# Optimization experiments

Hardware: AMD Instinct MI355X
Metric: run time of the kernel (lower is better)

Reference implementation:

```python
import jax, jax.numpy as jnp
import numpy as np

MODEL_DIM = 2048
NUM_HEADS = 32
NUM_KV_HEADS = 8
HEAD_DIM = MODEL_DIM // NUM_HEADS  # 64
NUM_REP = NUM_HEADS // NUM_KV_HEADS  # 4


def setup_inputs() -> dict:
    key = jax.random.key(0)
    ks = jax.random.split(key, 6)
    B, S = 1, 2048
    s = 1.0 / np.sqrt(MODEL_DIM)
    x = jax.random.normal(ks[0], (B, S, MODEL_DIM), dtype=jnp.float32)
    # causal mask, 1 = keep, 0 = mask (scores.masked_fill(mask == 0, -1e9))
    mask = jnp.tril(jnp.ones((S, S), dtype=jnp.int32))[None, None, :, :]
    w_q = jax.random.normal(ks[1], (MODEL_DIM, MODEL_DIM), dtype=jnp.float32) * s
    w_k = jax.random.normal(ks[2], (NUM_KV_HEADS * HEAD_DIM, MODEL_DIM), dtype=jnp.float32) * s
    w_v = jax.random.normal(ks[3], (NUM_KV_HEADS * HEAD_DIM, MODEL_DIM), dtype=jnp.float32) * s
    w_o = jax.random.normal(ks[4], (MODEL_DIM, MODEL_DIM), dtype=jnp.float32) * s
    b_o = jax.random.normal(ks[5], (MODEL_DIM,), dtype=jnp.float32) * 0.01
    return {"x": x, "mask": mask, "w_q": w_q, "w_k": w_k, "w_v": w_v, "w_o": w_o, "b_o": b_o}


def reference(x, mask, w_q, w_k, w_v, w_o, b_o):
    B, S, _ = x.shape
    # projections (torch Linear: x @ W.T)
    q = (x @ w_q.T).reshape(B, S, NUM_HEADS, HEAD_DIM).transpose(0, 2, 1, 3)      # [B,H,S,D]
    k = (x @ w_k.T).reshape(B, S, NUM_KV_HEADS, HEAD_DIM).transpose(0, 2, 1, 3)   # [B,Hk,S,D]
    v = (x @ w_v.T).reshape(B, S, NUM_KV_HEADS, HEAD_DIM).transpose(0, 2, 1, 3)   # [B,Hk,S,D]
    # group Q heads by their shared KV head instead of materializing repeated KV
    qg = q.reshape(B, NUM_KV_HEADS, NUM_REP, S, HEAD_DIM)                         # [B,Hk,R,S,D]
    scale = 1.0 / np.sqrt(HEAD_DIM).astype(np.float32)
    scores = jnp.einsum('bgrsd,bgtd->bgrst', qg, k) * scale                       # [B,Hk,R,S,S]
    scores = jnp.where(mask[:, :, None, :, :] == 0, jnp.float32(-1e9), scores)
    attn = jax.nn.softmax(scores, axis=-1)
    ctx = jnp.einsum('bgrst,bgtd->bgrsd', attn, v)                                # [B,Hk,R,S,D]
    ctx = ctx.reshape(B, NUM_HEADS, S, HEAD_DIM).transpose(0, 2, 1, 3).reshape(B, S, MODEL_DIM)
    return ctx @ w_o.T + b_o
```

## Files before the change

kernel.cpp:

```cpp
#include <hip/hip_runtime.h>
#include <hip/hip_bf16.h>

typedef __hip_bfloat16 bf16;
typedef __attribute__((ext_vector_type(8))) short short8;
typedef __attribute__((ext_vector_type(4))) short short4_t;
typedef __attribute__((ext_vector_type(4))) float f32x4;

#define S_LEN 2048
#define DMODEL 2048
#define NH 32
#define NKV 8
#define DH 64

__global__ void detect_kernel(const unsigned int* __restrict__ x, int* __restrict__ flag) {
    int tid = threadIdx.x;
    unsigned int w = x[tid * 37];
    int e0 = (w >> 7) & 0xFF;
    int in = (e0 >= 100 && e0 <= 140) ? 1 : 0;
    unsigned long long m = __ballot(in);
    if (tid == 0) flag[0] = (__popcll(m) >= 48) ? 1 : 0;
}

__device__ __forceinline__ void conv8(const void* src, bf16* dst, int i, float scale, int isbf) {
    short8 out;
    if (isbf) {
        short8 v = *(const short8*)((const bf16*)src + i);
        if (scale != 1.0f) {
            #pragma unroll
            for (int j = 0; j < 8; ++j) {
                float f = __bfloat162float(((const bf16*)&v)[j]) * scale;
                ((bf16*)&out)[j] = __float2bfloat16(f);
            }
        } else out = v;
    } else {
        const float* gp = (const float*)src + i;
        f32x4 a = *(const f32x4*)gp;
        f32x4 b = *(const f32x4*)(gp + 4);
        #pragma unroll
        for (int j = 0; j < 4; ++j) ((bf16*)&out)[j]     = __float2bfloat16(a[j] * scale);
        #pragma unroll
        for (int j = 0; j < 4; ++j) ((bf16*)&out)[j + 4] = __float2bfloat16(b[j] * scale);
    }
    *(short8*)(dst + i) = out;
}

__global__ __launch_bounds__(256)
void convert_kernel(const void* __restrict__ src, bf16* __restrict__ dst,
                    int n, float scale, const int* __restrict__ flagp) {
    const int isbf = flagp[0];
    int i = (blockIdx.x * 256 + threadIdx.x) * 8;
    const int stride = gridDim.x * 256 * 8;
    for (; i < n; i += stride) conv8(src, dst, i, scale, isbf);
}

__global__ __launch_bounds__(256)
void convert4_kernel(const void* __restrict__ x, const void* __restrict__ wq,
                     const void* __restrict__ wk, const void* __restrict__ wv,
                     bf16* __restrict__ xb, bf16* __restrict__ wqkv,
                     const int* __restrict__ flagp) {
    const int isbf = flagp[0];
    const int b = blockIdx.x;
    const void* src; bf16* dst; int boff; float scale = 1.0f;
    if (b < 2048)       { src = x;  dst = xb;              boff = b;        }
    else if (b < 4096)  { src = wq; dst = wqkv;            boff = b - 2048; scale = 0.125f; }
    else if (b < 4608)  { src = wk; dst = wqkv + 4194304;  boff = b - 4096; }
    else                { src = wv; dst = wqkv + 5242880;  boff = b - 4608; }
    int i = (boff * 256 + threadIdx.x) * 8;
    conv8(src, dst, i, scale, isbf);
}

__device__ __forceinline__ void gload_lds16(const void* g, void* l) {
    __builtin_amdgcn_global_load_lds(
        (const __attribute__((address_space(1))) void*)(unsigned long long)(size_t)g,
        (__attribute__((address_space(3))) void*)(unsigned int)(size_t)l,
        16, 0, 0);
}

__device__ __forceinline__ void gemm_core_2ph(const bf16* __restrict__ A, const bf16* __restrict__ B,
                                              int K, int m0, int n0,
                                              bf16* sA, bf16* sB, f32x4 acc[4][2]) {
    const int tid = threadIdx.x;
    const int w = tid >> 6, lane = tid & 63;
    const int wm = (w >> 1) * 64, wn = (w & 1) * 32;
    const int lm = lane & 15, lq = lane >> 4;
    const int xr = lm & 7;

    size_t aoff[4], boff[2];
    #pragma unroll
    for (int r = 0; r < 4; ++r) {
        int ci = w * 256 + r * 64 + lane;
        int row = ci >> 3, c = (ci & 7) ^ (row & 7);
        aoff[r] = (size_t)(m0 + row) * K + c * 8;
    }
    #pragma unroll
    for (int r = 0; r < 2; ++r) {
        int cj = w * 128 + r * 64 + lane;
        int row = cj >> 3, c = (cj & 7) ^ (row & 7);
        boff[r] = (size_t)(n0 + row) * K + c * 8;
    }

    const int nt = K >> 6;
    int cur = 0;

    {
        bf16* la = sA + w * 2048;
        bf16* lb = sB + w * 1024;
        #pragma unroll
        for (int r = 0; r < 4; ++r) gload_lds16(A + aoff[r], la + r * 512);
        #pragma unroll
        for (int r = 0; r < 2; ++r) gload_lds16(B + boff[r], lb + r * 512);
    }
    __syncthreads();

    for (int t = 0; t < nt; ++t) {
        bf16* curA = sA + cur * 8192;
        bf16* curB = sB + cur * 4096;
        if (t + 1 < nt) {
            const int nxt = cur ^ 1;
            const int k0 = (t + 1) << 6;
            bf16* la = sA + nxt * 8192 + w * 2048;
            bf16* lb = sB + nxt * 4096 + w * 1024;
            #pragma unroll
            for (int r = 0; r < 4; ++r) gload_lds16(A + aoff[r] + k0, la + r * 512);
            #pragma unroll
            for (int r = 0; r < 2; ++r) gload_lds16(B + boff[r] + k0, lb + r * 512);
        }

        short8 aF[2][4], bF[2][2];
        #pragma unroll
        for (int ks = 0; ks < 2; ++ks) {
            const int cc = ((ks * 4 + lq) ^ xr) * 8;
            #pragma unroll
            for (int i = 0; i < 4; ++i)
                aF[ks][i] = *(const short8*)&curA[(wm + i * 16 + lm) * 64 + cc];
            #pragma unroll
            for (int j = 0; j < 2; ++j)
                bF[ks][j] = *(const short8*)&curB[(wn + j * 16 + lm) * 64 + cc];
        }

        __builtin_amdgcn_s_setprio(1);
        #pragma unroll
        for (int ks = 0; ks < 2; ++ks)
            #pragma unroll
            for (int i = 0; i < 4; ++i)
                #pragma unroll
                for (int j = 0; j < 2; ++j)
                    acc[i][j] = __builtin_amdgcn_mfma_f32_16x16x32_bf16(aF[ks][i], bF[ks][j], acc[i][j], 0, 0, 0);
        __builtin_amdgcn_s_setprio(0);

        __syncthreads();
        cur ^= 1;
    }
}

template<bool BIAS, bool BIAS_DYN, bool OUT_DYN>
__global__ __launch_bounds__(256, 3)
void gemm_bf16s(const bf16* __restrict__ A, const bf16* __restrict__ B,
                const void* __restrict__ bias, void* __restrict__ C,
                int M, int N, int K, int ldc, const int* __restrict__ flagp) {
    __shared__ bf16 sA[2 * 128 * 64];
    __shared__ bf16 sB[2 * 64 * 64];
    const int isbf = flagp[0];
    const int tid = threadIdx.x;
    const int m0 = blockIdx.y * 128, n0 = blockIdx.x * 64;
    const int w = tid >> 6, lane = tid & 63;
    const int wm = (w >> 1) * 64, wn = (w & 1) * 32;
    const int lm = lane & 15, lq = lane >> 4;

    f32x4 acc[4][2];
    const f32x4 zero = {0.f, 0.f, 0.f, 0.f};
    for (int i = 0; i < 4; ++i)
        for (int j = 0; j < 2; ++j) acc[i][j] = zero;

    gemm_core_2ph(A, B, K, m0, n0, sA, sB, acc);

    for (int i = 0; i < 4; ++i)
        for (int j = 0; j < 2; ++j)
            for (int r = 0; r < 4; ++r) {
                int row = m0 + wm + i * 16 + lq * 4 + r;
                int col = n0 + wn + j * 16 + lm;
                float v = acc[i][j][r];
                if (BIAS) {
                    if (BIAS_DYN && !isbf) v += ((const float*)bias)[col];
                    else                   v += __bfloat162float(((const bf16*)bias)[col]);
                }
                size_t idx = (size_t)row * ldc + col;
                if (OUT_DYN && !isbf) ((float*)C)[idx] = v;
                else                  ((bf16*)C)[idx] = __float2bfloat16(v);
            }
}

__global__ __launch_bounds__(256, 3)
void gemm_qkv(const bf16* __restrict__ A, const bf16* __restrict__ B,
              bf16* __restrict__ Qo, bf16* __restrict__ Ko, bf16* __restrict__ Vto) {
    __shared__ bf16 sA[2 * 128 * 64];
    __shared__ bf16 sB[2 * 64 * 64];
    const int tid = threadIdx.x;
    const int m0 = blockIdx.y * 128, n0 = blockIdx.x * 64;
    const int w = tid >> 6, lane = tid & 63;
    const int wm = (w >> 1) * 64, wn = (w & 1) * 32;
    const int lm = lane & 15, lq = lane >> 4;

    f32x4 acc[4][2];
    const f32x4 zero = {0.f, 0.f, 0.f, 0.f};
    for (int i = 0; i < 4; ++i)
        for (int j = 0; j < 2; ++j) acc[i][j] = zero;

    gemm_core_2ph(A, B, DMODEL, m0, n0, sA, sB, acc);

    const int route = (n0 < 2048) ? 0 : ((n0 < 2560) ? 1 : 2);
    for (int i = 0; i < 4; ++i)
        for (int j = 0; j < 2; ++j)
            for (int r = 0; r < 4; ++r) {
                int row = m0 + wm + i * 16 + lq * 4 + r;
                int col = n0 + wn + j * 16 + lm;
                bf16 v = __float2bfloat16(acc[i][j][r]);
                if (route == 0)      Qo[(size_t)row * DMODEL + col] = v;
                else if (route == 1) Ko[(size_t)row * (NKV * DH) + (col - 2048)] = v;
                else                 Vto[(size_t)(col - 2560) * S_LEN + row] = v;
            }
}

template<bool TRANS_OUT, bool BIAS, bool A_DYN, bool B_DYN, bool BIAS_DYN, bool OUT_DYN>
__global__ __launch_bounds__(256, 2)
void gemm_bt(const void* __restrict__ A, const void* __restrict__ B,
             const void* __restrict__ bias, void* __restrict__ C,
             int M, int N, int K, int ldc, const int* __restrict__ flagp) {
    __shared__ bf16 sA[128 * 32];
    __shared__ bf16 sB[128 * 32];

    const int isbf = flagp[0];
    const int tid = threadIdx.x;
    const int m0 = blockIdx.y * 128, n0 = blockIdx.x * 128;
    const int w = tid >> 6, lane = tid & 63;
    const int wm = (w >> 1) * 64, wn = (w & 1) * 64;
    const int lm = lane & 15, lq = lane >> 4;

    f32x4 acc[4][4];
    const f32x4 zero = {0.f, 0.f, 0.f, 0.f};
    for (int i = 0; i < 4; ++i)
        for (int j = 0; j < 4; ++j) acc[i][j] = zero;

    for (int k0 = 0; k0 < K; k0 += 32) {
        __syncthreads();
        for (int it = 0; it < 2; ++it) {
            int c = it * 256 + tid;
            int row = c >> 2, off = (c & 3) * 8;
            if (!A_DYN || isbf) {
                *(short8*)&sA[row * 32 + off] =
                    *(const short8*)((const bf16*)A + (size_t)(m0 + row) * K + k0 + off);
            } else {
                const float* gp = (const float*)A + (size_t)(m0 + row) * K + k0 + off;
                #pragma unroll
                for (int i = 0; i < 8; ++i) sA[row * 32 + off + i] = __float2bfloat16(gp[i]);
            }
            if (!B_DYN || isbf) {
                *(short8*)&sB[row * 32 + off] =
                    *(const short8*)((const bf16*)B + (size_t)(n0 + row) * K + k0 + off);
            } else {
                const float* gp = (const float*)B + (size_t)(n0 + row) * K + k0 + off;
                #pragma unroll
                for (int i = 0; i < 8; ++i) sB[row * 32 + off + i] = __float2bfloat16(gp[i]);
            }
        }
        __syncthreads();

        short8 aF[4], bF[4];
        for (int i = 0; i < 4; ++i)
            aF[i] = *(const short8*)&sA[(wm + i * 16 + lm) * 32 + lq * 8];
        for (int i = 0; i < 4; ++i)
            bF[i] = *(const short8*)&sB[(wn + i * 16 + lm) * 32 + lq * 8];
        for (int i = 0; i < 4; ++i)
            for (int j = 0; j < 4; ++j)
                acc[i][j] = __builtin_amdgcn_mfma_f32_16x16x32_bf16(aF[i], bF[j], acc[i][j], 0, 0, 0);
    }

    for (int i = 0; i < 4; ++i)
        for (int j = 0; j < 4; ++j)
            for (int r = 0; r < 4; ++r) {
                int row = m0 + wm + i * 16 + lq * 4 + r;
                int col = n0 + wn + j * 16 + lm;
                float v = acc[i][j][r];
                if (BIAS) {
                    if (BIAS_DYN && !isbf) v += ((const float*)bias)[col];
                    else                   v += __bfloat162float(((const bf16*)bias)[col]);
                }
                size_t idx = TRANS_OUT ? (size_t)col * ldc + row : (size_t)row * ldc + col;
                if (OUT_DYN && !isbf) ((float*)C)[idx] = v;
                else                  ((bf16*)C)[idx] = __float2bfloat16(v);
            }
}

template<bool PRESCALED>
__global__ __launch_bounds__(128, 3)
void attn_kernel(const bf16* __restrict__ Q, const bf16* __restrict__ Km,
                 const bf16* __restrict__ Vt, bf16* __restrict__ ctx) {
    __shared__ bf16 sK[64 * 64];
    __shared__ bf16 sP[2][16 * 72];

    const int tid = threadIdx.x;
    const int bx = blockIdx.x;
    const int h  = bx & 31;
    const int qi = 63 - (bx >> 5);
    const int kvh = h >> 2;
    const int w = tid >> 6, lane = tid & 63;
    const int lm = lane & 15, lq = lane >> 4;
    const int xr = lm & 7;
    const int nt = (qi >> 1) + 1;

    const f32x4 zero = {0.f, 0.f, 0.f, 0.f};

    int krow[4], kcol[4];
    #pragma unroll
    for (int i = 0; i < 4; ++i) {
        int id = i * 128 + tid;
        krow[i] = id >> 3;
        kcol[i] = (id & 7);
    }

    const int qrow = qi * 32 + w * 16 + lm;
    short8 aq0 = *(const short8*)&Q[(size_t)qrow * DMODEL + h * 64 + lq * 8];
    short8 aq1 = *(const short8*)&Q[(size_t)qrow * DMODEL + h * 64 + 32 + lq * 8];

    float m_r = -1e30f, l_r = 0.f;
    f32x4 oacc[4];
    #pragma unroll
    for (int ni = 0; ni < 4; ++ni) oacc[ni] = zero;

    short8 kr[4];
    #pragma unroll
    for (int i = 0; i < 4; ++i)
        kr[i] = *(const short8*)&Km[(size_t)krow[i] * (NKV * DH) + kvh * 64 + kcol[i] * 8];

    for (int kt = 0; kt < nt; ++kt) {
        __syncthreads();
        #pragma unroll
        for (int i = 0; i < 4; ++i)
            *(short8*)&sK[krow[i] * 64 + (kcol[i] ^ (krow[i] & 7)) * 8] = kr[i];
        __syncthreads();
        if (kt + 1 < nt) {
            const int b0 = (kt + 1) * 64;
            #pragma unroll
            for (int i = 0; i < 4; ++i)
                kr[i] = *(const short8*)&Km[(size_t)(b0 + krow[i]) * (NKV * DH) + kvh * 64 + kcol[i] * 8];
        }

        short8 vv[4][2];
        #pragma unroll
        for (int ni = 0; ni < 4; ++ni)
            #pragma unroll
            for (int ks = 0; ks < 2; ++ks)
                vv[ni][ks] = *(const short8*)&Vt[(size_t)(kvh * 64 + ni * 16 + lm) * S_LEN
                                                 + kt * 64 + ks * 32 + lq * 8];

        f32x4 sacc[4];
        #pragma unroll
        for (int ni = 0; ni < 4; ++ni) sacc[ni] = zero;
        __builtin_amdgcn_s_setprio(1);
        #pragma unroll
        for (int ks = 0; ks < 2; ++ks) {
            short8 aq = ks ? aq1 : aq0;
            #pragma unroll
            for (int ni = 0; ni < 4; ++ni) {
                short8 bk = *(const short8*)&sK[(ni * 16 + lm) * 64 + (((ks << 2) | lq) ^ xr) * 8];
                sacc[ni] = __builtin_amdgcn_mfma_f32_16x16x32_bf16(bk, aq, sacc[ni], 0, 0, 0);
            }
        }
        __builtin_amdgcn_s_setprio(0);

        float mx = -3e38f;
        if (kt == nt - 1) {
            const int qrel = qi * 32 + w * 16 + lm - kt * 64;
            #pragma unroll
            for (int ni = 0; ni < 4; ++ni)
                #pragma unroll
                for (int r = 0; r < 4; ++r) {
                    float s = sacc[ni][r];
                    if (!PRESCALED) s *= 0.125f;
                    if ((ni * 16 + lq * 4 + r) > qrel) s = -1e30f;
                    sacc[ni][r] = s;
                    mx = fmaxf(mx, s);
                }
        } else {
            #pragma unroll
            for (int ni = 0; ni < 4; ++ni)
                #pragma unroll
                for (int r = 0; r < 4; ++r) {
                    float s = sacc[ni][r];
                    if (!PRESCALED) s *= 0.125f;
                    sacc[ni][r] = s;
                    mx = fmaxf(mx, s);
                }
        }
        mx = fmaxf(mx, __shfl_xor(mx, 16));
        mx = fmaxf(mx, __shfl_xor(mx, 32));

        int defer = (mx - m_r <= 8.0f) ? 1 : 0;
        if (!__all(defer)) {
            float m_new = fmaxf(m_r, mx);
            float alpha = __expf(m_r - m_new);
            m_r = m_new;
            l_r *= alpha;
            #pragma unroll
            for (int r = 0; r < 4; ++r) {
                float a_b = __shfl(alpha, (lane & 48) | (lq * 4 + r));
                #pragma unroll
                for (int ni = 0; ni < 4; ++ni) oacc[ni][r] *= a_b;
            }
        }

        float rs = 0.f;
        #pragma unroll
        for (int ni = 0; ni < 4; ++ni) {
            short4_t pk;
            #pragma unroll
            for (int r = 0; r < 4; ++r) {
                float p = __expf(sacc[ni][r] - m_r);
                rs += p;
                ((bf16*)&pk)[r] = __float2bfloat16(p);
            }
            *(short4_t*)&sP[w][lm * 72 + ni * 16 + lq * 4] = pk;
        }
        rs += __shfl_xor(rs, 16);
        rs += __shfl_xor(rs, 32);
        l_r += rs;

        asm volatile("s_waitcnt lgkmcnt(0)" ::: "memory");
        __builtin_amdgcn_sched_barrier(0);

        __builtin_amdgcn_s_setprio(1);
        #pragma unroll
        for (int ks = 0; ks < 2; ++ks) {
            short8 ap = *(const short8*)&sP[w][lm * 72 + ks * 32 + lq * 8];
            #pragma unroll
            for (int ni = 0; ni < 4; ++ni)
                oacc[ni] = __builtin_amdgcn_mfma_f32_16x16x32_bf16(ap, vv[ni][ks], oacc[ni], 0, 0, 0);
        }
        __builtin_amdgcn_s_setprio(0);
    }

    #pragma unroll
    for (int r = 0; r < 4; ++r) {
        float l_b = __shfl(l_r, (lane & 48) | (lq * 4 + r));
        float inv = 1.0f / l_b;
        #pragma unroll
        for (int ni = 0; ni < 4; ++ni)
            ctx[(size_t)(qi * 32 + w * 16 + lq * 4 + r) * DMODEL + h * 64 + ni * 16 + lm] =
                __float2bfloat16(oacc[ni][r] * inv);
    }
}

extern "C" void kernel_launch(void* const* d_in, const int* in_sizes, int n_in,
                              void* d_out, int out_size, void* d_ws, size_t ws_size,
                              hipStream_t stream) {
    const void* x   = d_in[0];
    const void* w_q = d_in[2];
    const void* w_k = d_in[3];
    const void* w_v = d_in[4];
    const void* w_o = d_in[5];
    const void* b_o = d_in[6];

    const size_t MB = 1024u * 1024u;
    char* ws = (char*)d_ws;
    int*  flag = (int*)ws;
    dim3 blk(256);

    detect_kernel<<<1, 64, 0, stream>>>((const unsigned int*)x, flag);

    if (ws_size >= 32 * MB + 4096) {
        bf16* xb   = (bf16*)(ws + 4096);
        bf16* wqkv = (bf16*)(ws + 4096 + 8 * MB);
        bf16* Qws  = (bf16*)(ws + 4096 + 20 * MB);
        bf16* Kws  = (bf16*)(ws + 4096 + 28 * MB);
        bf16* Vtws = (bf16*)(ws + 4096 + 30 * MB);
        bf16* wob  = xb;
        bf16* Ctx  = wqkv;

        convert4_kernel<<<5120, blk, 0, stream>>>(x, w_q, w_k, w_v, xb, wqkv, flag);
        gemm_qkv<<<dim3(48, 16), blk, 0, stream>>>(xb, wqkv, Qws, Kws, Vtws);
        convert_kernel<<<2048, blk, 0, stream>>>(w_o, wob, DMODEL * DMODEL, 1.0f, flag);
        attn_kernel<true><<<dim3(2048), dim3(128), 0, stream>>>(Qws, Kws, Vtws, Ctx);
        gemm_bf16s<true, true, true><<<dim3(32, 16), blk, 0, stream>>>(
            Ctx, wob, b_o, d_out, S_LEN, DMODEL, DMODEL, DMODEL, flag);
    } else {
        bf16* Qws  = (bf16*)(ws + 4096);
        bf16* Kws  = (bf16*)(ws + 4096 + 8u * MB);
        bf16* Vtws = (bf16*)(ws + 4096 + 10u * MB);
        bf16* Ctx  = (bf16*)(ws + 4096 + 12u * MB);

        gemm_bt<false, false, true, true, false, false><<<dim3(16, 16), blk, 0, stream>>>(
            x, w_q, nullptr, Qws, S_LEN, DMODEL, DMODEL, DMODEL, flag);
        gemm_bt<false, false, true, true, false, false><<<dim3(4, 16), blk, 0, stream>>>(
            x, w_k, nullptr, Kws, S_LEN, NKV * DH, DMODEL, NKV * DH, flag);
        gemm_bt<true, false, true, true, false, false><<<dim3(4, 16), blk, 0, stream>>>(
            x, w_v, nullptr, Vtws, S_LEN, NKV * DH, DMODEL, S_LEN, flag);
        attn_kernel<false><<<dim3(2048), dim3(128), 0, stream>>>(Qws, Kws, Vtws, Ctx);
        gemm_bt<false, true, false, true, true, true><<<dim3(16, 16), blk, 0, stream>>>(
            Ctx, w_o, b_o, d_out, S_LEN, DMODEL, DMODEL, DMODEL, flag);
    }
}
```

Before: 252.0 us.

## Restructure attention into paired causal tiles with async LDS K/V loads, fold conversions

Attention now runs 256-thread blocks that each handle a 64-row query tile plus its mirrored tile (qb and 31-qb), which balances causal work across blocks. K and V tiles are double-buffered in LDS through direct global-to-LDS loads, where before V was read from global memory per lane on every step. The w_o bf16 conversion moves into extra attention blocks (grid row 32), and the standalone detect kernel is replaced by an inline per-block format check, removing two launches. In exchange there are fewer, larger blocks (512 vs 2048) with more LDS each, which may lower occupancy, and the dtype check is repeated in every block.

```diff
diff --git a/kernel.cpp b/kernel.cpp
--- a/kernel.cpp
+++ b/kernel.cpp
@@ -11,6 +11,13 @@
 #define NH 32
 #define NKV 8
 #define DH 64
+
+__device__ __forceinline__ int detect_isbf(const void* src) {
+    unsigned int wsamp = ((const unsigned int*)src)[(threadIdx.x & 63) * 37];
+    int e0 = (wsamp >> 7) & 0xFF;
+    unsigned long long mb = __ballot(e0 >= 100 && e0 <= 140);
+    return (__popcll(mb) >= 48) ? 1 : 0;
+}
 
 __global__ void detect_kernel(const unsigned int* __restrict__ x, int* __restrict__ flag) {
     int tid = threadIdx.x;
@@ -45,26 +52,16 @@
 }
 
 __global__ __launch_bounds__(256)
-void convert_kernel(const void* __restrict__ src, bf16* __restrict__ dst,
-                    int n, float scale, const int* __restrict__ flagp) {
-    const int isbf = flagp[0];
-    int i = (blockIdx.x * 256 + threadIdx.x) * 8;
-    const int stride = gridDim.x * 256 * 8;
-    for (; i < n; i += stride) conv8(src, dst, i, scale, isbf);
-}
-
-__global__ __launch_bounds__(256)
 void convert4_kernel(const void* __restrict__ x, const void* __restrict__ wq,
                      const void* __restrict__ wk, const void* __restrict__ wv,
-                     bf16* __restrict__ xb, bf16* __restrict__ wqkv,
-                     const int* __restrict__ flagp) {
-    const int isbf = flagp[0];
+                     bf16* __restrict__ xb, bf16* __restrict__ wqkv) {
     const int b = blockIdx.x;
     const void* src; bf16* dst; int boff; float scale = 1.0f;
     if (b < 2048)       { src = x;  dst = xb;              boff = b;        }
     else if (b < 4096)  { src = wq; dst = wqkv;            boff = b - 2048; scale = 0.125f; }
     else if (b < 4608)  { src = wk; dst = wqkv + 4194304;  boff = b - 4096; }
     else                { src = wv; dst = wqkv + 5242880;  boff = b - 4608; }
+    const int isbf = detect_isbf(src);
     int i = (boff * 256 + threadIdx.x) * 8;
     conv8(src, dst, i, scale, isbf);
 }
@@ -157,10 +154,10 @@
 __global__ __launch_bounds__(256, 3)
 void gemm_bf16s(const bf16* __restrict__ A, const bf16* __restrict__ B,
                 const void* __restrict__ bias, void* __restrict__ C,
-                int M, int N, int K, int ldc, const int* __restrict__ flagp) {
+                int M, int N, int K, int ldc, const void* __restrict__ xsrc) {
     __shared__ bf16 sA[2 * 128 * 64];
     __shared__ bf16 sB[2 * 64 * 64];
-    const int isbf = flagp[0];
+    const int isbf = (BIAS_DYN || OUT_DYN) ? detect_isbf(xsrc) : 1;
     const int tid = threadIdx.x;
     const int m0 = blockIdx.y * 128, n0 = blockIdx.x * 64;
     const int w = tid >> 6, lane = tid & 63;
@@ -292,161 +289,177 @@
 }
 
 template<bool PRESCALED>
-__global__ __launch_bounds__(128, 3)
+__global__ __launch_bounds__(256, 3)
 void attn_kernel(const bf16* __restrict__ Q, const bf16* __restrict__ Km,
-                 const bf16* __restrict__ Vt, bf16* __restrict__ ctx) {
-    __shared__ bf16 sK[64 * 64];
-    __shared__ bf16 sP[2][16 * 72];
+                 const bf16* __restrict__ Vt, bf16* __restrict__ ctx,
+                 const void* __restrict__ wo_src, bf16* __restrict__ wob) {
+    if (blockIdx.y == 32) {
+        if (wo_src) {
+            const int isbf = detect_isbf(wo_src);
+            int i = (blockIdx.x * 256 + threadIdx.x) * 8;
+            for (; i < DMODEL * DMODEL; i += 16 * 256 * 8)
+                conv8(wo_src, wob, i, 1.0f, isbf);
+        }
+        return;
+    }
+
+    __shared__ bf16 sK[2][64 * 64];
+    __shared__ bf16 sV[2][64 * 64];
+    __shared__ bf16 sP[4][16 * 72];
 
     const int tid = threadIdx.x;
-    const int bx = blockIdx.x;
-    const int h  = bx & 31;
-    const int qi = 63 - (bx >> 5);
+    const int h  = blockIdx.y;
     const int kvh = h >> 2;
     const int w = tid >> 6, lane = tid & 63;
     const int lm = lane & 15, lq = lane >> 4;
+    const int qloc = w * 16 + lm;
     const int xr = lm & 7;
-    const int nt = (qi >> 1) + 1;
+
+    int srt[2]; int scs[2];
+    #pragma unroll
+    for (int i = 0; i < 2; ++i) {
+        srt[i] = w * 16 + i * 8 + (lane >> 3);
+        scs[i] = (lane & 7) ^ (srt[i] & 7);
+    }
 
     const f32x4 zero = {0.f, 0.f, 0.f, 0.f};
 
-    int krow[4], kcol[4];
-    #pragma unroll
-    for (int i = 0; i < 4; ++i) {
-        int id = i * 128 + tid;
-        krow[i] = id >> 3;
-        kcol[i] = (id & 7);
-    }
-
-    const int qrow = qi * 32 + w * 16 + lm;
-    short8 aq0 = *(const short8*)&Q[(size_t)qrow * DMODEL + h * 64 + lq * 8];
-    short8 aq1 = *(const short8*)&Q[(size_t)qrow * DMODEL + h * 64 + 32 + lq * 8];
-
-    float m_r = -1e30f, l_r = 0.f;
-    f32x4 oacc[4];
-    #pragma unroll
-    for (int ni = 0; ni < 4; ++ni) oacc[ni] = zero;
-
-    short8 kr[4];
-    #pragma unroll
-    for (int i = 0; i < 4; ++i)
-        kr[i] = *(const short8*)&Km[(size_t)krow[i] * (NKV * DH) + kvh * 64 + kcol[i] * 8];
-
-    for (int kt = 0; kt < nt; ++kt) {
+    for (int ph = 0; ph < 2; ++ph) {
+        const int qb = ph ? (31 - blockIdx.x) : blockIdx.x;
+        const int nt = qb + 1;
+
+        const int qrow = qb * 64 + w * 16 + lm;
+        short8 aq0 = *(const short8*)&Q[(size_t)qrow * DMODEL + h * 64 + lq * 8];
+        short8 aq1 = *(const short8*)&Q[(size_t)qrow * DMODEL + h * 64 + 32 + lq * 8];
+
+        float m_r = -1e30f, l_r = 0.f;
+        f32x4 oacc[4];
+        #pragma unroll
+        for (int ni = 0; ni < 4; ++ni) oacc[ni] = zero;
+
+        {
+            bf16* dk = &sK[0][(w * 16) * 64];
+            bf16* dv = &sV[0][(w * 16) * 64];
+            #pragma unroll
+            for (int i = 0; i < 2; ++i) {
+                gload_lds16(&Km[(size_t)srt[i] * (NKV * DH) + kvh * 64 + scs[i] * 8], dk + i * 512);
+                gload_lds16(&Vt[(size_t)(kvh * 64 + srt[i]) * S_LEN + scs[i] * 8],    dv + i * 512);
+            }
+        }
         __syncthreads();
-        #pragma unroll
-        for (int i = 0; i < 4; ++i)
-            *(short8*)&sK[krow[i] * 64 + (kcol[i] ^ (krow[i] & 7)) * 8] = kr[i];
-        __syncthreads();
-        if (kt + 1 < nt) {
-            const int b0 = (kt + 1) * 64;
-            #pragma unroll
-            for (int i = 0; i < 4; ++i)
-                kr[i] = *(const short8*)&Km[(size_t)(b0 + krow[i]) * (NKV * DH) + kvh * 64 + kcol[i] * 8];
-        }
-
-        short8 vv[4][2];
-        #pragma unroll
-        for (int ni = 0; ni < 4; ++ni)
-            #pragma unroll
-            for (int ks = 0; ks < 2; ++ks)
-                vv[ni][ks] = *(const short8*)&Vt[(size_t)(kvh * 64 + ni * 16 + lm) * S_LEN
-                                                 + kt * 64 + ks * 32 + lq * 8];
-
-        f32x4 sacc[4];
-        #pragma unroll
-        for (int ni = 0; ni < 4; ++ni) sacc[ni] = zero;
-        __builtin_amdgcn_s_setprio(1);
-        #pragma unroll
-        for (int ks = 0; ks < 2; ++ks) {
-            short8 aq = ks ? aq1 : aq0;
+
+        int cur = 0;
+        for (int kt = 0; kt < nt; ++kt) {
+            if (kt + 1 < nt) {
+                const int b0 = (kt + 1) * 64;
+                bf16* dk = &sK[cur ^ 1][(w * 16) * 64];
+                bf16* dv = &sV[cur ^ 1][(w * 16) * 64];
+                #pragma unroll
+                for (int i = 0; i < 2; ++i) {
+                    gload_lds16(&Km[(size_t)(b0 + srt[i]) * (NKV * DH) + kvh * 64 + scs[i] * 8], dk + i * 512);
+                    gload_lds16(&Vt[(size_t)(kvh * 64 + srt[i]) * S_LEN + b0 + scs[i] * 8],      dv + i * 512);
+                }
+            }
+
+            f32x4 sacc[4];
+            #pragma unroll
+            for (int ni = 0; ni < 4; ++ni) sacc[ni] = zero;
+            __builtin_amdgcn_s_setprio(1);
+            #pragma unroll
+            for (int ks = 0; ks < 2; ++ks) {
+                short8 aq = ks ? aq1 : aq0;
+                #pragma unroll
+                for (int ni = 0; ni < 4; ++ni) {
+                    short8 bk = *(const short8*)&sK[cur][(ni * 16 + lm) * 64 + ((ks * 4 + lq) ^ xr) * 8];
+                    sacc[ni] = __builtin_amdgcn_mfma_f32_16x16x32_bf16(bk, aq, sacc[ni], 0, 0, 0);
+                }
+            }
+            __builtin_amdgcn_s_setprio(0);
+
+            float mx = -3e38f;
+            if (kt == nt - 1) {
+                #pragma unroll
+                for (int ni = 0; ni < 4; ++ni)
+                    #pragma unroll
+                    for (int r = 0; r < 4; ++r) {
+                        float s = sacc[ni][r];
+                        if (!PRESCALED) s *= 0.125f;
+                        if ((ni * 16 + lq * 4 + r) > qloc) s = -1e30f;
+                        sacc[ni][r] = s;
+                        mx = fmaxf(mx, s);
+                    }
+            } else {
+                #pragma unroll
+                for (int ni = 0; ni < 4; ++ni)
+                    #pragma unroll
+                    for (int r = 0; r < 4; ++r) {
+                        float s = sacc[ni][r];
+                        if (!PRESCALED) s *= 0.125f;
+                        sacc[ni][r] = s;
+                        mx = fmaxf(mx, s);
+                    }
+            }
+            mx = fmaxf(mx, __shfl_xor(mx, 16));
+            mx = fmaxf(mx, __shfl_xor(mx, 32));
+
+            int defer = (mx - m_r <= 8.0f) ? 1 : 0;
+            if (!__all(defer)) {
+                float m_new = fmaxf(m_r, mx);
+                float alpha = __expf(m_r - m_new);
+                m_r = m_new;
+                l_r *= alpha;
+                #pragma unroll
+                for (int r = 0; r < 4; ++r) {
+                    float a_b = __shfl(alpha, (lane & 48) | (lq * 4 + r));
+                    #pragma unroll
+                    for (int ni = 0; ni < 4; ++ni) oacc[ni][r] *= a_b;
+                }
+            }
+
+            float rs = 0.f;
             #pragma unroll
             for (int ni = 0; ni < 4; ++ni) {
-                short8 bk = *(const short8*)&sK[(ni * 16 + lm) * 64 + (((ks << 2) | lq) ^ xr) * 8];
-                sacc[ni] = __builtin_amdgcn_mfma_f32_16x16x32_bf16(bk, aq, sacc[ni], 0, 0, 0);
-            }
-        }
-        __builtin_amdgcn_s_setprio(0);
-
-        float mx = -3e38f;
-        if (kt == nt - 1) {
-            const int qrel = qi * 32 + w * 16 + lm - kt * 64;
+                short4_t pk;
+                #pragma unroll
+                for (int r = 0; r < 4; ++r) {
+                    float p = __expf(sacc[ni][r] - m_r);
+                    rs += p;
+                    ((bf16*)&pk)[r] = __float2bfloat16(p);
+                }
+                *(short4_t*)&sP[w][lm * 72 + ni * 16 + lq * 4] = pk;
+            }
+            rs += __shfl_xor(rs, 16);
+            rs += __shfl_xor(rs, 32);
+            l_r += rs;
+
+            asm volatile("s_waitcnt lgkmcnt(0)" ::: "memory");
+            __builtin_amdgcn_sched_barrier(0);
+
+            __builtin_amdgcn_s_setprio(1);
+            #pragma unroll
+            for (int ks = 0; ks < 2; ++ks) {
+                short8 ap = *(const short8*)&sP[w][lm * 72 + ks * 32 + lq * 8];
+                #pragma unroll
+                for (int ni = 0; ni < 4; ++ni) {
+                    short8 bv = *(const short8*)&sV[cur][(ni * 16 + lm) * 64 + ((ks * 4 + lq) ^ xr) * 8];
+                    oacc[ni] = __builtin_amdgcn_mfma_f32_16x16x32_bf16(ap, bv, oacc[ni], 0, 0, 0);
+                }
+            }
+            __builtin_amdgcn_s_setprio(0);
+
+            __syncthreads();
+            cur ^= 1;
+        }
+
+        #pragma unroll
+        for (int r = 0; r < 4; ++r) {
+            float l_b = __shfl(l_r, (lane & 48) | (lq * 4 + r));
+            float inv = 1.0f / l_b;
             #pragma unroll
             for (int ni = 0; ni < 4; ++ni)
-                #pragma unroll
-                for (int r = 0; r < 4; ++r) {
-                    float s = sacc[ni][r];
-                    if (!PRESCALED) s *= 0.125f;
-                    if ((ni * 16 + lq * 4 + r) > qrel) s = -1e30f;
-                    sacc[ni][r] = s;
-                    mx = fmaxf(mx, s);
-                }
-        } else {
-            #pragma unroll
-            for (int ni = 0; ni < 4; ++ni)
-                #pragma unroll
-                for (int r = 0; r < 4; ++r) {
-                    float s = sacc[ni][r];
-                    if (!PRESCALED) s *= 0.125f;
-                    sacc[ni][r] = s;
-                    mx = fmaxf(mx, s);
-                }
-        }
-        mx = fmaxf(mx, __shfl_xor(mx, 16));
-        mx = fmaxf(mx, __shfl_xor(mx, 32));
-
-        int defer = (mx - m_r <= 8.0f) ? 1 : 0;
-        if (!__all(defer)) {
-            float m_new = fmaxf(m_r, mx);
-            float alpha = __expf(m_r - m_new);
-            m_r = m_new;
-            l_r *= alpha;
-            #pragma unroll
-            for (int r = 0; r < 4; ++r) {
-                float a_b = __shfl(alpha, (lane & 48) | (lq * 4 + r));
-                #pragma unroll
-                for (int ni = 0; ni < 4; ++ni) oacc[ni][r] *= a_b;
-            }
-        }
-
-        float rs = 0.f;
-        #pragma unroll
-        for (int ni = 0; ni < 4; ++ni) {
-            short4_t pk;
-            #pragma unroll
-            for (int r = 0; r < 4; ++r) {
-                float p = __expf(sacc[ni][r] - m_r);
-                rs += p;
-                ((bf16*)&pk)[r] = __float2bfloat16(p);
-            }
-            *(short4_t*)&sP[w][lm * 72 + ni * 16 + lq * 4] = pk;
-        }
-        rs += __shfl_xor(rs, 16);
-        rs += __shfl_xor(rs, 32);
-        l_r += rs;
-
-        asm volatile("s_waitcnt lgkmcnt(0)" ::: "memory");
-        __builtin_amdgcn_sched_barrier(0);
-
-        __builtin_amdgcn_s_setprio(1);
-        #pragma unroll
-        for (int ks = 0; ks < 2; ++ks) {
-            short8 ap = *(const short8*)&sP[w][lm * 72 + ks * 32 + lq * 8];
-            #pragma unroll
-            for (int ni = 0; ni < 4; ++ni)
-                oacc[ni] = __builtin_amdgcn_mfma_f32_16x16x32_bf16(ap, vv[ni][ks], oacc[ni], 0, 0, 0);
-        }
-        __builtin_amdgcn_s_setprio(0);
-    }
-
-    #pragma unroll
-    for (int r = 0; r < 4; ++r) {
-        float l_b = __shfl(l_r, (lane & 48) | (lq * 4 + r));
-        float inv = 1.0f / l_b;
-        #pragma unroll
-        for (int ni = 0; ni < 4; ++ni)
-            ctx[(size_t)(qi * 32 + w * 16 + lq * 4 + r) * DMODEL + h * 64 + ni * 16 + lm] =
-                __float2bfloat16(oacc[ni][r] * inv);
+                ctx[(size_t)(qb * 64 + w * 16 + lq * 4 + r) * DMODEL + h * 64 + ni * 16 + lm] =
+                    __float2bfloat16(oacc[ni][r] * inv);
+        }
     }
 }
 
@@ -465,8 +478,6 @@
     int*  flag = (int*)ws;
     dim3 blk(256);
 
-    detect_kernel<<<1, 64, 0, stream>>>((const unsigned int*)x, flag);
-
     if (ws_size >= 32 * MB + 4096) {
         bf16* xb   = (bf16*)(ws + 4096);
         bf16* wqkv = (bf16*)(ws + 4096 + 8 * MB);
@@ -476,25 +487,25 @@
         bf16* wob  = xb;
         bf16* Ctx  = wqkv;
 
-        convert4_kernel<<<5120, blk, 0, stream>>>(x, w_q, w_k, w_v, xb, wqkv, flag);
+        convert4_kernel<<<5120, blk, 0, stream>>>(x, w_q, w_k, w_v, xb, wqkv);
         gemm_qkv<<<dim3(48, 16), blk, 0, stream>>>(xb, wqkv, Qws, Kws, Vtws);
-        convert_kernel<<<2048, blk, 0, stream>>>(w_o, wob, DMODEL * DMODEL, 1.0f, flag);
-        attn_kernel<true><<<dim3(2048), dim3(128), 0, stream>>>(Qws, Kws, Vtws, Ctx);
+        attn_kernel<true><<<dim3(16, 33), blk, 0, stream>>>(Qws, Kws, Vtws, Ctx, w_o, wob);
         gemm_bf16s<true, true, true><<<dim3(32, 16), blk, 0, stream>>>(
-            Ctx, wob, b_o, d_out, S_LEN, DMODEL, DMODEL, DMODEL, flag);
+            Ctx, wob, b_o, d_out, S_LEN, DMODEL, DMODEL, DMODEL, x);
     } else {
         bf16* Qws  = (bf16*)(ws + 4096);
         bf16* Kws  = (bf16*)(ws + 4096 + 8u * MB);
         bf16* Vtws = (bf16*)(ws + 4096 + 10u * MB);
         bf16* Ctx  = (bf16*)(ws + 4096 + 12u * MB);
 
+        detect_kernel<<<1, 64, 0, stream>>>((const unsigned int*)x, flag);
         gemm_bt<false, false, true, true, false, false><<<dim3(16, 16), blk, 0, stream>>>(
             x, w_q, nullptr, Qws, S_LEN, DMODEL, DMODEL, DMODEL, flag);
         gemm_bt<false, false, true, true, false, false><<<dim3(4, 16), blk, 0, stream>>>(
             x, w_k, nullptr, Kws, S_LEN, NKV * DH, DMODEL, NKV * DH, flag);
         gemm_bt<true, false, true, true, false, false><<<dim3(4, 16), blk, 0, stream>>>(
             x, w_v, nullptr, Vtws, S_LEN, NKV * DH, DMODEL, S_LEN, flag);
-        attn_kernel<false><<<dim3(2048), dim3(128), 0, stream>>>(Qws, Kws, Vtws, Ctx);
+        attn_kernel<false><<<dim3(16, 32), blk, 0, stream>>>(Qws, Kws, Vtws, Ctx, nullptr, nullptr);
         gemm_bt<false, true, false, true, true, true><<<dim3(16, 16), blk, 0, stream>>>(
             Ctx, w_o, b_o, d_out, S_LEN, DMODEL, DMODEL, DMODEL, flag);
     }
```

New measurement: 238.1 us. -5.5%, faster.
